# Performance work log

Hardware: AMD Instinct MI355X
Metric: run time of the kernel (lower is better)

The kernel has to match this reference:

```python
import jax, jax.numpy as jnp
import numpy as np

B, C, H, W = 4, 512, 128, 128
CI = C // 2   # inter_planes
CQ = C // 8   # q/k dim in CrossAttention


def conv1x1(x, w, b=None):
    # x: [B,Cin,H,W], w: [Cout,Cin]
    y = jnp.einsum('oc,bchw->bohw', w, x)
    if b is not None:
        y = y + b[None, :, None, None]
    return y


def setup_inputs() -> dict:
    key = jax.random.key(0)
    ks = jax.random.split(key, 13)
    s = 0.05
    return {
        'x': jax.random.normal(ks[0], (B, C, H, W), jnp.float32),
        # SCCA gating params (1x1 convs, no bias except conv_up)
        'w_q_right': jax.random.normal(ks[1], (1, C), jnp.float32) * s,
        'w_v_right': jax.random.normal(ks[2], (CI, C), jnp.float32) * s,
        'w_up': jax.random.normal(ks[3], (C, CI), jnp.float32) * s,
        'b_up': jnp.zeros((C,), jnp.float32),
        'w_q_left': jax.random.normal(ks[4], (CI, C), jnp.float32) * s,
        'w_v_left': jax.random.normal(ks[5], (CI, C), jnp.float32) * s,
        # CrossAttention params (1x1 convs with bias)
        'wq': jax.random.normal(ks[6], (CQ, C), jnp.float32) * s,
        'bq': jnp.zeros((CQ,), jnp.float32),
        'wk': jax.random.normal(ks[7], (CQ, C), jnp.float32) * s,
        'bk': jnp.zeros((CQ,), jnp.float32),
        'wv': jax.random.normal(ks[8], (C, C), jnp.float32) * s,
        'bv': jnp.zeros((C,), jnp.float32),
        'gamma': jnp.asarray(0.5, jnp.float32),
    }


def cross_attention(x, wq, bq, wk, bk, wv, bv, gamma):
    # criss-cross attention: each pixel attends to its row and column
    b, c, h, w = x.shape
    q = conv1x1(x, wq, bq)   # [B,CQ,H,W]
    k = conv1x1(x, wk, bk)   # [B,CQ,H,W]
    v = conv1x1(x, wv, bv)   # [B,C,H,W]
    # column (H) affinities with -inf on the self diagonal (as in INF())
    diag = jnp.where(jnp.eye(h, dtype=bool), -jnp.inf, 0.0).astype(x.dtype)
    e_h = jnp.einsum('bchw,bcgw->bhwg', q, k) + diag[None, :, None, :]  # [B,H,W,H]
    e_w = jnp.einsum('bchw,bchv->bhwv', q, k)                            # [B,H,W,W]
    att = jax.nn.softmax(jnp.concatenate([e_h, e_w], axis=-1), axis=-1)  # [B,H,W,H+W]
    a_h, a_w = att[..., :h], att[..., h:]
    out_h = jnp.einsum('bcgw,bhwg->bchw', v, a_h)
    out_w = jnp.einsum('bchv,bhwv->bchw', v, a_w)
    return gamma * (out_h + out_w) + x


def spatial_weighted(x, w_q_right, w_v_right, w_up, b_up):
    b, c, h, w = x.shape
    input_x = conv1x1(x, w_v_right).reshape(b, CI, h * w)       # [B,CI,HW]
    mask = jax.nn.softmax(conv1x1(x, w_q_right).reshape(b, h * w), axis=-1)  # [B,HW]
    ctx = jnp.einsum('bcn,bn->bc', input_x, mask)               # [B,CI]
    ctx = jnp.einsum('oc,bc->bo', w_up, ctx) + b_up             # [B,C]
    mask_ch = jax.nn.sigmoid(ctx)[:, :, None, None]
    return x * mask_ch


def channel_weighted(x, w_q_left, w_v_left):
    b, c, h, w = x.shape
    g_x = conv1x1(x, w_q_left)                                  # [B,CI,H,W]
    avg = g_x.mean(axis=(2, 3))                                 # [B,CI]
    theta = conv1x1(x, w_v_left).reshape(b, CI, h * w)          # [B,CI,HW]
    ctx = jax.nn.softmax(jnp.einsum('bc,bcn->bn', avg, theta), axis=-1)
    mask_sp = jax.nn.sigmoid(ctx).reshape(b, 1, h, w)
    return x * mask_sp


def reference(x, w_q_right, w_v_right, w_up, b_up, w_q_left, w_v_left,
              wq, bq, wk, bk, wv, bv, gamma):
    cc = spatial_weighted(x, w_q_right, w_v_right, w_up, b_up)
    cc = cross_attention(cc, wq, bq, wk, bk, wv, bv, gamma)
    cs = channel_weighted(x, w_q_left, w_v_left)
    cs = cross_attention(cs, wq, bq, wk, bk, wv, bv, gamma)
    out = cs + cc
    out = cross_attention(out, wq, bq, wk, bk, wv, bv, gamma)
    return out
```

## Files before the change

kernel.cpp:

```cpp
#include <hip/hip_runtime.h>
#include <hip/hip_bf16.h>
#include <math.h>

typedef __hip_bfloat16 bf16;
typedef __attribute__((ext_vector_type(8))) short s16x8;
typedef __attribute__((ext_vector_type(4))) float f32x4;

constexpr int Bn  = 4;
constexpr int Cn  = 512;
constexpr int Hn  = 128;
constexpr int Wn  = 128;
constexpr int Nn  = Hn * Wn;
constexpr int CQn = 64;
constexpr int CIn = 256;

__device__ __forceinline__ float bf2f(bf16 v){ return __bfloat162float(v); }
__device__ __forceinline__ bf16  f2bf(float v){ return __float2bfloat16(v); }

__device__ __forceinline__ void gload_lds16(const void* g, void* l){
  __builtin_amdgcn_global_load_lds(
      (const __attribute__((address_space(1))) unsigned int*)g,
      (__attribute__((address_space(3))) unsigned int*)l,
      16, 0, 0);
}


__global__ __launch_bounds__(256) void k_dotc2(const float* __restrict__ x,
                                               const float* __restrict__ w,
                                               int wstride,
                                               float* __restrict__ part){
  int t = blockIdx.x * 256 + threadIdx.x;
  int half = blockIdx.y;
  int b = t >> 14;
  const float* wp = w + (size_t)b * wstride + half * 256;
  const float* xp = x + (size_t)b * Cn * Nn + (size_t)(half * 256) * Nn + (t & (Nn - 1));
  float acc = 0.f;
  #pragma unroll 16
  for (int c = 0; c < 256; ++c) acc += wp[c] * xp[(size_t)c * Nn];
  part[(size_t)half * (Bn * Nn) + t] = acc;
}

__global__ __launch_bounds__(256) void k_dotcadd(const float* __restrict__ part,
                                                 float* __restrict__ out){
  int t = blockIdx.x * 256 + threadIdx.x;
  out[t] = part[t] + part[(size_t)Bn * Nn + t];
}

__global__ __launch_bounds__(256) void k_rowmean(const float* __restrict__ x,
                                                 float* __restrict__ out,
                                                 float scale){
  int bc = blockIdx.x;
  const float* xp = x + (size_t)bc * Nn;
  float acc = 0.f;
  for (int n = threadIdx.x; n < Nn; n += 256) acc += xp[n];
  for (int o = 32; o > 0; o >>= 1) acc += __shfl_down(acc, o);
  __shared__ float red[4];
  if ((threadIdx.x & 63) == 0) red[threadIdx.x >> 6] = acc;
  __syncthreads();
  if (threadIdx.x == 0) out[bc] = (red[0] + red[1] + red[2] + red[3]) * scale;
}

__global__ __launch_bounds__(256) void k_rowdot(const float* __restrict__ W,
                                                const float* __restrict__ vec,
                                                float* __restrict__ out){
  __shared__ float vs[Cn];
  int b = blockIdx.x, t = threadIdx.x;
  for (int j = t; j < Cn; j += 256) vs[j] = vec[b * Cn + j];
  __syncthreads();
  const float4* wp = (const float4*)(W + (size_t)t * Cn);
  float a = 0.f;
  #pragma unroll 4
  for (int j = 0; j < Cn / 4; ++j){
    float4 w4 = wp[j];
    a += w4.x * vs[4*j] + w4.y * vs[4*j+1] + w4.z * vs[4*j+2] + w4.w * vs[4*j+3];
  }
  out[b * CIn + t] = a;
}

__global__ __launch_bounds__(256) void k_coldot(const float* __restrict__ W,
                                                const float* __restrict__ vec,
                                                float* __restrict__ out){
  __shared__ float vs[CIn];
  int b = blockIdx.y, t = threadIdx.x;
  int c = blockIdx.x * 256 + t;
  if (t < CIn) vs[t] = vec[b * CIn + t];
  __syncthreads();
  float a = 0.f;
  #pragma unroll 8
  for (int j = 0; j < CIn; ++j) a += W[(size_t)j * Cn + c] * vs[j];
  out[b * Cn + c] = a;
}

__global__ __launch_bounds__(256) void k_mch2(const float* __restrict__ w_up,
                                              const float* __restrict__ b_up,
                                              const float* __restrict__ ctx,
                                              float* __restrict__ mch){
  __shared__ float cs[CIn];
  int b = blockIdx.y, t = threadIdx.x;
  int o = blockIdx.x * 256 + t;
  if (t < CIn) cs[t] = ctx[b * CIn + t];
  __syncthreads();
  const float4* wp = (const float4*)(w_up + (size_t)o * CIn);
  float a = b_up[o];
  #pragma unroll 4
  for (int j = 0; j < CIn / 4; ++j){
    float4 w4 = wp[j];
    a += w4.x * cs[4*j] + w4.y * cs[4*j+1] + w4.z * cs[4*j+2] + w4.w * cs[4*j+3];
  }
  mch[b * Cn + o] = 1.f / (1.f + expf(-a));
}

__global__ __launch_bounds__(1024) void k_stats(const float* __restrict__ vv,
                                                float* __restrict__ stats){
  int b = blockIdx.x;
  const float* pp = vv + (size_t)b * Nn;
  int t = threadIdx.x;
  float m = -3.4e38f;
  for (int n = t; n < Nn; n += 1024) m = fmaxf(m, pp[n]);
  for (int o = 32; o > 0; o >>= 1) m = fmaxf(m, __shfl_down(m, o));
  __shared__ float red[16];
  int wid = t >> 6, lid = t & 63;
  if (lid == 0) red[wid] = m;
  __syncthreads();
  if (t == 0){
    float q = red[0];
    for (int i = 1; i < 16; i++) q = fmaxf(q, red[i]);
    red[0] = q;
  }
  __syncthreads();
  m = red[0];
  __syncthreads();
  float s = 0.f;
  for (int n = t; n < Nn; n += 1024) s += expf(pp[n] - m);
  for (int o = 32; o > 0; o >>= 1) s += __shfl_down(s, o);
  if (lid == 0) red[wid] = s;
  __syncthreads();
  if (t == 0){
    float q = 0.f;
    for (int i = 0; i < 16; i++) q += red[i];
    stats[b * 2]     = m;
    stats[b * 2 + 1] = q;
  }
}

__global__ __launch_bounds__(256) void k_weighted(const float* __restrict__ x,
                                                  const float* __restrict__ logits,
                                                  const float* __restrict__ stats,
                                                  float* __restrict__ out){
  int bc = blockIdx.x;
  int b = bc >> 9;
  const float* xp = x + (size_t)bc * Nn;
  const float* lp = logits + (size_t)b * Nn;
  float m = stats[b * 2], den = stats[b * 2 + 1];
  float acc = 0.f;
  for (int n = threadIdx.x; n < Nn; n += 256) acc += xp[n] * expf(lp[n] - m);
  for (int o = 32; o > 0; o >>= 1) acc += __shfl_down(acc, o);
  __shared__ float red[4];
  if ((threadIdx.x & 63) == 0) red[threadIdx.x >> 6] = acc;
  __syncthreads();
  if (threadIdx.x == 0) out[bc] = (red[0] + red[1] + red[2] + red[3]) / den;
}

__global__ __launch_bounds__(256) void k_msp(const float* __restrict__ lg,
                                             const float* __restrict__ stats,
                                             float* __restrict__ msp){
  int t = blockIdx.x * 256 + threadIdx.x;
  int b = t >> 14;
  float v = expf(lg[t] - stats[b * 2]) / stats[b * 2 + 1];
  msp[t] = 1.f / (1.f + expf(-v));
}

__global__ __launch_bounds__(256) void k_applyT3(const float* __restrict__ x,
                                                 const float* __restrict__ mch,
                                                 const float* __restrict__ msp,
                                                 bf16* __restrict__ cc_hi,
                                                 bf16* __restrict__ cc_lo,
                                                 bf16* __restrict__ cs_hi,
                                                 bf16* __restrict__ cs_lo){
  __shared__ bf16 tch[32][33], tcl[32][33], tsh[32][33], tsl[32][33];
  int nt = blockIdx.x, ct = blockIdx.y, b = blockIdx.z;
  int n0 = nt * 32, c0 = ct * 32;
  int t = threadIdx.x;
  #pragma unroll
  for (int kk = 0; kk < 4; ++kk){
    int idx = t + kk * 256;
    int cl = idx >> 5, nl = idx & 31;
    float xv = x[((size_t)(b * Cn + c0 + cl)) * Nn + n0 + nl];
    float ccv = xv * mch[b * Cn + c0 + cl];
    float csv = xv * msp[b * Nn + n0 + nl];
    bf16 h1 = f2bf(ccv);
    tch[cl][nl] = h1;
    tcl[cl][nl] = f2bf(ccv - bf2f(h1));
    bf16 h2 = f2bf(csv);
    tsh[cl][nl] = h2;
    tsl[cl][nl] = f2bf(csv - bf2f(h2));
  }
  __syncthreads();
  #pragma unroll
  for (int kk = 0; kk < 4; ++kk){
    int idx = t + kk * 256;
    int nl = idx >> 5, cl = idx & 31;
    size_t o = ((size_t)(b * Nn + n0 + nl)) * Cn + c0 + cl;
    cc_hi[o] = tch[cl][nl];
    cc_lo[o] = tcl[cl][nl];
    cs_hi[o] = tsh[cl][nl];
    cs_lo[o] = tsl[cl][nl];
  }
}


__global__ __launch_bounds__(256) void k_cvt_w(const float* __restrict__ in,
                                               bf16* __restrict__ out, int n){
  int t = blockIdx.x * 256 + threadIdx.x;
  if (t < n) out[t] = f2bf(in[t]);
}

__global__ __launch_bounds__(256) void k_prep_wqk(const float* __restrict__ wq,
                                                  const float* __restrict__ wk,
                                                  const float* __restrict__ bq,
                                                  const float* __restrict__ bk,
                                                  bf16* __restrict__ wqk_hi,
                                                  bf16* __restrict__ wqk_lo,
                                                  float* __restrict__ bqk){
  int t = blockIdx.x * 256 + threadIdx.x;
  int o = t >> 9, c = t & 511;
  float v = (o < 64) ? wq[(size_t)o * Cn + c] : wk[(size_t)(o - 64) * Cn + c];
  bf16 h = f2bf(v);
  wqk_hi[t] = h;
  wqk_lo[t] = f2bf(v - bf2f(h));
  if (t < 128) bqk[t] = (t < 64) ? bq[t] : bk[t - 64];
}

__global__ __launch_bounds__(256) void k_cvt_T(const float* __restrict__ in,
                                               bf16* __restrict__ out_hi,
                                               bf16* __restrict__ out_lo){
  __shared__ bf16 th_[32][33];
  __shared__ bf16 tl_[32][33];
  int nt = blockIdx.x, ct = blockIdx.y, b = blockIdx.z;
  int n0 = nt * 32, c0 = ct * 32;
  int t = threadIdx.x;
  #pragma unroll
  for (int kk = 0; kk < 4; ++kk){
    int idx = t + kk * 256;
    int cl = idx >> 5, nl = idx & 31;
    float v = in[((size_t)(b * Cn + c0 + cl)) * Nn + n0 + nl];
    bf16 h = f2bf(v);
    th_[cl][nl] = h;
    tl_[cl][nl] = f2bf(v - bf2f(h));
  }
  __syncthreads();
  #pragma unroll
  for (int kk = 0; kk < 4; ++kk){
    int idx = t + kk * 256;
    int nl = idx >> 5, cl = idx & 31;
    size_t o = ((size_t)(b * Nn + n0 + nl)) * Cn + c0 + cl;
    out_hi[o] = th_[cl][nl];
    out_lo[o] = tl_[cl][nl];
  }
}


__global__ __launch_bounds__(256) void k_v_mfma(const bf16* __restrict__ xT,
                                                const bf16* __restrict__ wvb,
                                                const float* __restrict__ bv,
                                                bf16* __restrict__ v){
  __shared__ short As[128 * 64];
  __shared__ short Bs[128 * 64];
  __shared__ float bvs[128];
  int lin = blockIdx.x;
  int swz = (lin & 7) * 256 + (lin >> 3);
  int cb = (swz & 3) * 128;
  int nb = ((swz >> 2) & 127) * 128;
  int b  = swz >> 9;
  int t = threadIdx.x, lane = t & 63, wid = t >> 6;
  int wm = wid >> 1, wn = wid & 1;
  int l15 = lane & 15, l4 = lane >> 4;
  if (t < 128) bvs[t] = bv[cb + t];
  f32x4 acc[4][4];
  #pragma unroll
  for (int i = 0; i < 4; i++)
    #pragma unroll
    for (int j = 0; j < 4; j++) acc[i][j] = (f32x4){0.f, 0.f, 0.f, 0.f};

  const bf16* wp = wvb + (size_t)cb * Cn;
  const bf16* xp = xT + ((size_t)b * Nn + nb) * Cn;
  int r8 = lane >> 3;
  int kc = (lane & 7) * 8;
  for (int kt = 0; kt < 8; ++kt){
    int k0 = kt * 64;
    #pragma unroll
    for (int j = 0; j < 4; ++j){
      int inst = wid * 4 + j;
      int row = inst * 8 + r8;
      gload_lds16(wp + (size_t)row * Cn + k0 + kc, (char*)As + inst * 1024);
      gload_lds16(xp + (size_t)row * Cn + k0 + kc, (char*)Bs + inst * 1024);
    }
    __syncthreads();
    #pragma unroll
    for (int kk = 0; kk < 64; kk += 32){
      s16x8 a[4], bb[4];
      #pragma unroll
      for (int mi = 0; mi < 4; mi++)
        a[mi] = *(const s16x8*)&As[(wm * 64 + mi * 16 + l15) * 64 + kk + l4 * 8];
      #pragma unroll
      for (int ni = 0; ni < 4; ni++)
        bb[ni] = *(const s16x8*)&Bs[(wn * 64 + ni * 16 + l15) * 64 + kk + l4 * 8];
      #pragma unroll
      for (int mi = 0; mi < 4; mi++)
        #pragma unroll
        for (int ni = 0; ni < 4; ni++)
          acc[mi][ni] = __builtin_amdgcn_mfma_f32_16x16x32_bf16(a[mi], bb[ni], acc[mi][ni], 0, 0, 0);
    }
    __syncthreads();
  }
  #pragma unroll
  for (int mi = 0; mi < 4; mi++){
    #pragma unroll
    for (int r = 0; r < 4; r++){
      int cl = wm * 64 + mi * 16 + l4 * 4 + r;
      int c  = cb + cl;
      float bias = bvs[cl];
      #pragma unroll
      for (int ni = 0; ni < 4; ni++){
        int n = nb + wn * 64 + ni * 16 + l15;
        v[((size_t)(b * Cn + c)) * Nn + n] = f2bf(acc[mi][ni][r] + bias);
      }
    }
  }
}

__global__ __launch_bounds__(256) void k_qk_mfma(const bf16* __restrict__ xT_hi,
                                                 const bf16* __restrict__ xT_lo,
                                                 const bf16* __restrict__ wqk_hi,
                                                 const bf16* __restrict__ wqk_lo,
                                                 const float* __restrict__ bqk,
                                                 bf16* __restrict__ qhw,
                                                 bf16* __restrict__ khw){
  __shared__ char smem[65536];
  short* Ah = (short*)smem;
  short* Al = Ah + 8192;
  short* Bh = Al + 8192;
  short* Bl = Bh + 8192;
  char*  Os = smem;
  __shared__ float bs[128];
  int h = blockIdx.x, b = blockIdx.y;
  int nb = h * 128;
  int t = threadIdx.x, lane = t & 63, wid = t >> 6;
  int wm = wid >> 1, wn = wid & 1;
  int l15 = lane & 15, l4 = lane >> 4;
  if (t < 128) bs[t] = bqk[t];
  f32x4 acc[4][4];
  #pragma unroll
  for (int i = 0; i < 4; i++)
    #pragma unroll
    for (int j = 0; j < 4; j++) acc[i][j] = (f32x4){0.f, 0.f, 0.f, 0.f};

  const bf16* xh = xT_hi + ((size_t)b * Nn + nb) * Cn;
  const bf16* xl = xT_lo + ((size_t)b * Nn + nb) * Cn;
  int r8 = lane >> 3;
  int kc = (lane & 7) * 8;
  for (int kt = 0; kt < 8; ++kt){
    int k0 = kt * 64;
    #pragma unroll
    for (int j = 0; j < 4; ++j){
      int inst = wid * 4 + j;
      int row = inst * 8 + r8;
      size_t off = (size_t)row * Cn + k0 + kc;
      gload_lds16(wqk_hi + off, (char*)Ah + inst * 1024);
      gload_lds16(wqk_lo + off, (char*)Al + inst * 1024);
      gload_lds16(xh + off,     (char*)Bh + inst * 1024);
      gload_lds16(xl + off,     (char*)Bl + inst * 1024);
    }
    __syncthreads();
    #pragma unroll
    for (int kk = 0; kk < 64; kk += 32){
      s16x8 ah[4], al[4], bh[4], bl[4];
      #pragma unroll
      for (int mi = 0; mi < 4; mi++){
        int idx = (wm * 64 + mi * 16 + l15) * 64 + kk + l4 * 8;
        ah[mi] = *(const s16x8*)&Ah[idx];
        al[mi] = *(const s16x8*)&Al[idx];
      }
      #pragma unroll
      for (int ni = 0; ni < 4; ni++){
        int idx = (wn * 64 + ni * 16 + l15) * 64 + kk + l4 * 8;
        bh[ni] = *(const s16x8*)&Bh[idx];
        bl[ni] = *(const s16x8*)&Bl[idx];
      }
      #pragma unroll
      for (int mi = 0; mi < 4; mi++)
        #pragma unroll
        for (int ni = 0; ni < 4; ni++){
          acc[mi][ni] = __builtin_amdgcn_mfma_f32_16x16x32_bf16(ah[mi], bh[ni], acc[mi][ni], 0, 0, 0);
          acc[mi][ni] = __builtin_amdgcn_mfma_f32_16x16x32_bf16(ah[mi], bl[ni], acc[mi][ni], 0, 0, 0);
          acc[mi][ni] = __builtin_amdgcn_mfma_f32_16x16x32_bf16(al[mi], bh[ni], acc[mi][ni], 0, 0, 0);
        }
    }
    __syncthreads();
  }
  #pragma unroll
  for (int mi = 0; mi < 4; mi++){
    #pragma unroll
    for (int r = 0; r < 4; r++){
      int o = wm * 64 + mi * 16 + l4 * 4 + r;
      float bias = bs[o];
      #pragma unroll
      for (int ni = 0; ni < 4; ni++){
        int n = wn * 64 + ni * 16 + l15;
        bf16 bv = f2bf(acc[mi][ni][r] + bias);
        int byte = (n * 256 + o * 2) ^ ((n & 7) << 4);
        *(unsigned short*)(Os + byte) = *(unsigned short*)&bv;
      }
    }
  }
  __syncthreads();
  #pragma unroll
  for (int i = 0; i < 8; ++i){
    int s = t + i * 256;
    int row = s >> 3, seg = s & 7;
    int w = row & 127, qk = row >> 7;
    int o0 = qk * 64 + seg * 8;
    int byte = (w * 256 + o0 * 2) ^ ((w & 7) << 4);
    s16x8 d = *(const s16x8*)(Os + byte);
    bf16* dst = (qk == 0 ? qhw : khw) + (((size_t)b * Wn + w) * Hn + h) * CQn + seg * 8;
    *(s16x8*)dst = d;
  }
}


__global__ __launch_bounds__(256) void k_att_h(const bf16* __restrict__ qhw,
                                               const bf16* __restrict__ khw,
                                               const bf16* __restrict__ vT,
                                               float* __restrict__ mh,
                                               float* __restrict__ sh,
                                               bf16* __restrict__ ohX){
  __shared__ char smem[65536];
  char* attb = smem;
  char* vbb  = smem + 32768;
  float* redm = (float*)(smem + 32768);
  float* reds = redm + 256;
  int w = blockIdx.x, b = blockIdx.y;
  int t = threadIdx.x, lane = t & 63, wid = t >> 6;
  int wm = wid >> 1, wn = wid & 1;
  int l15 = lane & 15, l4 = lane >> 4;

  const bf16* qp = qhw + ((size_t)(b * Wn + w)) * (Hn * CQn);
  const bf16* kp = khw + ((size_t)(b * Wn + w)) * (Hn * CQn);
  f32x4 acc[4][4];
  #pragma unroll
  for (int i = 0; i < 4; i++)
    #pragma unroll
    for (int j = 0; j < 4; j++) acc[i][j] = (f32x4){0.f, 0.f, 0.f, 0.f};
  #pragma unroll
  for (int kk = 0; kk < 64; kk += 32){
    s16x8 a[4], bb[4];
    #pragma unroll
    for (int mi = 0; mi < 4; mi++)
      a[mi] = *(const s16x8*)(qp + (size_t)(wm * 64 + mi * 16 + l15) * CQn + kk + l4 * 8);
    #pragma unroll
    for (int ni = 0; ni < 4; ni++)
      bb[ni] = *(const s16x8*)(kp + (size_t)(wn * 64 + ni * 16 + l15) * CQn + kk + l4 * 8);
    #pragma unroll
    for (int mi = 0; mi < 4; mi++)
      #pragma unroll
      for (int ni = 0; ni < 4; ni++)
        acc[mi][ni] = __builtin_amdgcn_mfma_f32_16x16x32_bf16(a[mi], bb[ni], acc[mi][ni], 0, 0, 0);
  }
  if (wm == wn){
    #pragma unroll
    for (int mi = 0; mi < 4; mi++)
      #pragma unroll
      for (int r = 0; r < 4; r++)
        if (l15 == l4 * 4 + r) acc[mi][mi][r] = -1e30f;
  }
  float rm[4][4];
  #pragma unroll
  for (int mi = 0; mi < 4; mi++)
    #pragma unroll
    for (int r = 0; r < 4; r++){
      float m = fmaxf(fmaxf(acc[mi][0][r], acc[mi][1][r]),
                      fmaxf(acc[mi][2][r], acc[mi][3][r]));
      m = fmaxf(m, __shfl_xor(m, 1));
      m = fmaxf(m, __shfl_xor(m, 2));
      m = fmaxf(m, __shfl_xor(m, 4));
      m = fmaxf(m, __shfl_xor(m, 8));
      rm[mi][r] = m;
    }
  if (l15 == 0){
    #pragma unroll
    for (int mi = 0; mi < 4; mi++)
      #pragma unroll
      for (int r = 0; r < 4; r++)
        redm[wn * 128 + wm * 64 + mi * 16 + l4 * 4 + r] = rm[mi][r];
  }
  __syncthreads();
  float rs[4][4];
  #pragma unroll
  for (int mi = 0; mi < 4; mi++)
    #pragma unroll
    for (int r = 0; r < 4; r++){
      int h = wm * 64 + mi * 16 + l4 * 4 + r;
      float m = fmaxf(redm[h], redm[128 + h]);
      rm[mi][r] = m;
      float s = 0.f;
      #pragma unroll
      for (int ni = 0; ni < 4; ni++){
        acc[mi][ni][r] = expf(acc[mi][ni][r] - m);
        s += acc[mi][ni][r];
      }
      s += __shfl_xor(s, 1);
      s += __shfl_xor(s, 2);
      s += __shfl_xor(s, 4);
      s += __shfl_xor(s, 8);
      rs[mi][r] = s;
    }
  if (l15 == 0){
    #pragma unroll
    for (int mi = 0; mi < 4; mi++)
      #pragma unroll
      for (int r = 0; r < 4; r++)
        reds[wn * 128 + wm * 64 + mi * 16 + l4 * 4 + r] = rs[mi][r];
  }
  __syncthreads();
  #pragma unroll
  for (int mi = 0; mi < 4; mi++)
    #pragma unroll
    for (int r = 0; r < 4; r++){
      int h = wm * 64 + mi * 16 + l4 * 4 + r;
      if (wn == 0 && l15 == 0){
        mh[(size_t)(b * Wn + w) * Hn + h] = rm[mi][r];
        sh[(size_t)(b * Wn + w) * Hn + h] = reds[h] + reds[128 + h];
      }
      #pragma unroll
      for (int ni = 0; ni < 4; ni++){
        int g = wn * 64 + ni * 16 + l15;
        bf16 bv = f2bf(acc[mi][ni][r]);
        int byte = (h * 256 + g * 2) ^ ((h & 7) << 4);
        *(unsigned short*)(attb + byte) = *(unsigned short*)&bv;
      }
    }
  __syncthreads();
  for (int cb = 0; cb < Cn; cb += 128){
    const bf16* vp = vT + ((size_t)(b * Wn + w) * Cn + cb) * Hn;
    for (int s = t; s < 2048; s += 256){
      int row = s >> 4, seg = s & 15;
      s16x8 d = *(const s16x8*)(vp + (size_t)row * Hn + seg * 8);
      int byte = (row * 256 + seg * 16) ^ ((row & 7) << 4);
      *(s16x8*)(vbb + byte) = d;
    }
    __syncthreads();
    f32x4 acc2[4][4];
    #pragma unroll
    for (int i = 0; i < 4; i++)
      #pragma unroll
      for (int j = 0; j < 4; j++) acc2[i][j] = (f32x4){0.f, 0.f, 0.f, 0.f};
    #pragma unroll
    for (int kk = 0; kk < 128; kk += 32){
      s16x8 a[4], bb[4];
      #pragma unroll
      for (int mi = 0; mi < 4; mi++){
        int row = wm * 64 + mi * 16 + l15;
        int byte = (row * 256 + (kk + l4 * 8) * 2) ^ ((row & 7) << 4);
        a[mi] = *(const s16x8*)(vbb + byte);
      }
      #pragma unroll
      for (int ni = 0; ni < 4; ni++){
        int row = wn * 64 + ni * 16 + l15;
        int byte = (row * 256 + (kk + l4 * 8) * 2) ^ ((row & 7) << 4);
        bb[ni] = *(const s16x8*)(attb + byte);
      }
      #pragma unroll
      for (int mi = 0; mi < 4; mi++)
        #pragma unroll
        for (int ni = 0; ni < 4; ni++)
          acc2[mi][ni] = __builtin_amdgcn_mfma_f32_16x16x32_bf16(a[mi], bb[ni], acc2[mi][ni], 0, 0, 0);
    }
    bf16* op = ohX + ((size_t)(b * Cn + cb)) * Nn + (size_t)w * Hn;
    #pragma unroll
    for (int mi = 0; mi < 4; mi++)
      #pragma unroll
      for (int r = 0; r < 4; r++){
        int cl = wm * 64 + mi * 16 + l4 * 4 + r;
        #pragma unroll
        for (int ni = 0; ni < 4; ni++){
          int h = wn * 64 + ni * 16 + l15;
          op[(size_t)cl * Nn + h] = f2bf(acc2[mi][ni][r]);
        }
      }
    __syncthreads();
  }
}

__global__ __launch_bounds__(256) void k_att_w(const bf16* __restrict__ qhw,
                                               const bf16* __restrict__ khw,
                                               const bf16* __restrict__ v,
                                               float* __restrict__ mw,
                                               float* __restrict__ sw,
                                               bf16* __restrict__ ow){
  __shared__ char smem[65536];
  char* attb = smem;
  char* vbb  = smem + 32768;
  float* redm = (float*)(smem + 32768);
  float* reds = redm + 256;
  int h = blockIdx.x, b = blockIdx.y;
  int t = threadIdx.x, lane = t & 63, wid = t >> 6;
  int wm = wid >> 1, wn = wid & 1;
  int l15 = lane & 15, l4 = lane >> 4;

  const bf16* qp = qhw + (size_t)b * Wn * Hn * CQn + (size_t)h * CQn;
  const bf16* kp = khw + (size_t)b * Wn * Hn * CQn + (size_t)h * CQn;
  f32x4 acc[4][4];
  #pragma unroll
  for (int i = 0; i < 4; i++)
    #pragma unroll
    for (int j = 0; j < 4; j++) acc[i][j] = (f32x4){0.f, 0.f, 0.f, 0.f};
  #pragma unroll
  for (int kk = 0; kk < 64; kk += 32){
    s16x8 a[4], bb[4];
    #pragma unroll
    for (int mi = 0; mi < 4; mi++)
      a[mi] = *(const s16x8*)(qp + (size_t)(wm * 64 + mi * 16 + l15) * (Hn * CQn) + kk + l4 * 8);
    #pragma unroll
    for (int ni = 0; ni < 4; ni++)
      bb[ni] = *(const s16x8*)(kp + (size_t)(wn * 64 + ni * 16 + l15) * (Hn * CQn) + kk + l4 * 8);
    #pragma unroll
    for (int mi = 0; mi < 4; mi++)
      #pragma unroll
      for (int ni = 0; ni < 4; ni++)
        acc[mi][ni] = __builtin_amdgcn_mfma_f32_16x16x32_bf16(a[mi], bb[ni], acc[mi][ni], 0, 0, 0);
  }
  float rm[4][4];
  #pragma unroll
  for (int mi = 0; mi < 4; mi++)
    #pragma unroll
    for (int r = 0; r < 4; r++){
      float m = fmaxf(fmaxf(acc[mi][0][r], acc[mi][1][r]),
                      fmaxf(acc[mi][2][r], acc[mi][3][r]));
      m = fmaxf(m, __shfl_xor(m, 1));
      m = fmaxf(m, __shfl_xor(m, 2));
      m = fmaxf(m, __shfl_xor(m, 4));
      m = fmaxf(m, __shfl_xor(m, 8));
      rm[mi][r] = m;
    }
  if (l15 == 0){
    #pragma unroll
    for (int mi = 0; mi < 4; mi++)
      #pragma unroll
      for (int r = 0; r < 4; r++)
        redm[wn * 128 + wm * 64 + mi * 16 + l4 * 4 + r] = rm[mi][r];
  }
  __syncthreads();
  float rs[4][4];
  #pragma unroll
  for (int mi = 0; mi < 4; mi++)
    #pragma unroll
    for (int r = 0; r < 4; r++){
      int wr = wm * 64 + mi * 16 + l4 * 4 + r;
      float m = fmaxf(redm[wr], redm[128 + wr]);
      rm[mi][r] = m;
      float s = 0.f;
      #pragma unroll
      for (int ni = 0; ni < 4; ni++){
        acc[mi][ni][r] = expf(acc[mi][ni][r] - m);
        s += acc[mi][ni][r];
      }
      s += __shfl_xor(s, 1);
      s += __shfl_xor(s, 2);
      s += __shfl_xor(s, 4);
      s += __shfl_xor(s, 8);
      rs[mi][r] = s;
    }
  if (l15 == 0){
    #pragma unroll
    for (int mi = 0; mi < 4; mi++)
      #pragma unroll
      for (int r = 0; r < 4; r++)
        reds[wn * 128 + wm * 64 + mi * 16 + l4 * 4 + r] = rs[mi][r];
  }
  __syncthreads();
  #pragma unroll
  for (int mi = 0; mi < 4; mi++)
    #pragma unroll
    for (int r = 0; r < 4; r++){
      int wr = wm * 64 + mi * 16 + l4 * 4 + r;
      if (wn == 0 && l15 == 0){
        mw[(size_t)(b * Hn + h) * Wn + wr] = rm[mi][r];
        sw[(size_t)(b * Hn + h) * Wn + wr] = reds[wr] + reds[128 + wr];
      }
      #pragma unroll
      for (int ni = 0; ni < 4; ni++){
        int g = wn * 64 + ni * 16 + l15;
        bf16 bv = f2bf(acc[mi][ni][r]);
        int byte = (wr * 256 + g * 2) ^ ((wr & 7) << 4);
        *(unsigned short*)(attb + byte) = *(unsigned short*)&bv;
      }
    }
  __syncthreads();
  for (int cb = 0; cb < Cn; cb += 128){
    const bf16* vp = v + (size_t)(b * Cn + cb) * Nn + (size_t)h * Wn;
    for (int s = t; s < 2048; s += 256){
      int row = s >> 4, seg = s & 15;
      s16x8 d = *(const s16x8*)(vp + (size_t)row * Nn + seg * 8);
      int byte = (row * 256 + seg * 16) ^ ((row & 7) << 4);
      *(s16x8*)(vbb + byte) = d;
    }
    __syncthreads();
    f32x4 acc2[4][4];
    #pragma unroll
    for (int i = 0; i < 4; i++)
      #pragma unroll
      for (int j = 0; j < 4; j++) acc2[i][j] = (f32x4){0.f, 0.f, 0.f, 0.f};
    #pragma unroll
    for (int kk = 0; kk < 128; kk += 32){
      s16x8 a[4], bb[4];
      #pragma unroll
      for (int mi = 0; mi < 4; mi++){
        int row = wm * 64 + mi * 16 + l15;
        int byte = (row * 256 + (kk + l4 * 8) * 2) ^ ((row & 7) << 4);
        a[mi] = *(const s16x8*)(vbb + byte);
      }
      #pragma unroll
      for (int ni = 0; ni < 4; ni++){
        int row = wn * 64 + ni * 16 + l15;
        int byte = (row * 256 + (kk + l4 * 8) * 2) ^ ((row & 7) << 4);
        bb[ni] = *(const s16x8*)(attb + byte);
      }
      #pragma unroll
      for (int mi = 0; mi < 4; mi++)
        #pragma unroll
        for (int ni = 0; ni < 4; ni++)
          acc2[mi][ni] = __builtin_amdgcn_mfma_f32_16x16x32_bf16(a[mi], bb[ni], acc2[mi][ni], 0, 0, 0);
    }
    bf16* op = ow + (size_t)(b * Cn + cb) * Nn + (size_t)h * Wn;
    #pragma unroll
    for (int mi = 0; mi < 4; mi++)
      #pragma unroll
      for (int r = 0; r < 4; r++){
        int cl = wm * 64 + mi * 16 + l4 * 4 + r;
        #pragma unroll
        for (int ni = 0; ni < 4; ni++){
          int wr = wn * 64 + ni * 16 + l15;
          op[(size_t)cl * Nn + wr] = f2bf(acc2[mi][ni][r]);
        }
      }
    __syncthreads();
  }
}

__global__ __launch_bounds__(256) void k_alpha(const float* __restrict__ mh,
                                               const float* __restrict__ sh,
                                               const float* __restrict__ mw,
                                               const float* __restrict__ sw,
                                               float* __restrict__ ahT,
                                               float* __restrict__ aw){
  int t = blockIdx.x * 256 + threadIdx.x;
  int b = t >> 14;
  int hw = t & (Nn - 1);
  int h = hw >> 7, w = hw & 127;
  size_t ih = (size_t)(b * Wn + w) * Hn + h;
  size_t iw = t;
  float mhv = mh[ih], mwv = mw[iw];
  float M = fmaxf(mhv, mwv);
  float eh_ = expf(mhv - M), ew_ = expf(mwv - M);
  float inv = 1.f / (sh[ih] * eh_ + sw[iw] * ew_);
  ahT[t] = eh_ * inv;
  aw[t]  = ew_ * inv;
}


__global__ __launch_bounds__(256) void k_trans(const bf16* __restrict__ in,
                                               bf16* __restrict__ out,
                                               int CH){
  __shared__ bf16 tile[32][33];
  int tl = blockIdx.x, c = blockIdx.y, b = blockIdx.z;
  int th = tl >> 2, tw = tl & 3;
  int h0 = th * 32, w0 = tw * 32;
  int t = threadIdx.x;
  const bf16* ip = in + ((size_t)(b * CH + c)) * Nn;
  #pragma unroll
  for (int kk = 0; kk < 4; ++kk){
    int idx = t + kk * 256;
    int hl = idx >> 5, wl = idx & 31;
    tile[hl][wl] = ip[(h0 + hl) * Wn + w0 + wl];
  }
  __syncthreads();
  #pragma unroll
  for (int kk = 0; kk < 4; ++kk){
    int idx = t + kk * 256;
    int wl = idx >> 5, hl = idx & 31;
    out[((size_t)(b * Wn + w0 + wl) * CH + c) * Hn + h0 + hl] = tile[hl][wl];
  }
}

__global__ __launch_bounds__(256) void k_fuse2(const float* __restrict__ in,
                                               const bf16* __restrict__ ohX,
                                               const bf16* __restrict__ ow,
                                               const float* __restrict__ ahT,
                                               const float* __restrict__ aw,
                                               const float* __restrict__ gamma,
                                               float* __restrict__ out){
  __shared__ unsigned short tileT[64][138];
  int c = blockIdx.x, half = blockIdx.y, b = blockIdx.z;
  int t = threadIdx.x;
  float g = gamma[0];
  int h0 = half * 64;
  const bf16* ohp = ohX + ((size_t)(b * Cn + c)) * Nn;
  #pragma unroll
  for (int i = 0; i < 4; ++i){
    int s = t + i * 256;
    int w = s >> 3, seg = s & 7;
    s16x8 d = *(const s16x8*)(ohp + (size_t)w * Hn + h0 + seg * 8);
    #pragma unroll
    for (int j = 0; j < 8; ++j)
      tileT[seg * 8 + j][w] = (unsigned short)d[j];
  }
  __syncthreads();
  size_t base = ((size_t)(b * Cn + c)) * Nn;
  #pragma unroll
  for (int i = 0; i < 8; ++i){
    int o = t + i * 256;
    int hl = o >> 5, w4 = (o & 31) * 4;
    int h = h0 + hl;
    size_t idx = base + (size_t)h * Wn + w4;
    size_t aidx = (size_t)b * Nn + (size_t)h * Wn + w4;
    ushort4 owv = *(const ushort4*)((const unsigned short*)ow + idx);
    float4 ah4 = *(const float4*)(ahT + aidx);
    float4 aw4 = *(const float4*)(aw + aidx);
    float4 inv = in ? *(const float4*)(in + idx) : (float4){0.f,0.f,0.f,0.f};
    float r[4];
    #pragma unroll
    for (int j = 0; j < 4; ++j){
      unsigned short uh = tileT[hl][w4 + j];
      unsigned short uo = ((const unsigned short*)&owv)[j];
      float ohv = bf2f(*(bf16*)&uh);
      float owf = bf2f(*(bf16*)&uo);
      float ahv = ((const float*)&ah4)[j];
      float awv = ((const float*)&aw4)[j];
      r[j] = g * (ahv * ohv + awv * owf) + ((const float*)&inv)[j];
    }
    float4 o4 = { r[0], r[1], r[2], r[3] };
    *(float4*)(out + idx) = o4;
  }
}

__global__ __launch_bounds__(256) void k_fuse3(const float* __restrict__ x,
                                               const float* __restrict__ mch,
                                               const float* __restrict__ msp,
                                               const bf16* __restrict__ oh1,
                                               const bf16* __restrict__ ow1,
                                               const float* __restrict__ a1h,
                                               const float* __restrict__ a1w,
                                               const bf16* __restrict__ oh2,
                                               const bf16* __restrict__ ow2,
                                               const float* __restrict__ a2h,
                                               const float* __restrict__ a2w,
                                               const float* __restrict__ gamma,
                                               float* __restrict__ out){
  __shared__ unsigned short t1[64][138];
  __shared__ unsigned short t2[64][138];
  int c = blockIdx.x, half = blockIdx.y, b = blockIdx.z;
  int t = threadIdx.x;
  float g = gamma[0];
  float mc = mch[b * Cn + c];
  int h0 = half * 64;
  const bf16* p1 = oh1 + ((size_t)(b * Cn + c)) * Nn;
  const bf16* p2 = oh2 + ((size_t)(b * Cn + c)) * Nn;
  #pragma unroll
  for (int i = 0; i < 4; ++i){
    int s = t + i * 256;
    int w = s >> 3, seg = s & 7;
    s16x8 d1 = *(const s16x8*)(p1 + (size_t)w * Hn + h0 + seg * 8);
    s16x8 d2 = *(const s16x8*)(p2 + (size_t)w * Hn + h0 + seg * 8);
    #pragma unroll
    for (int j = 0; j < 8; ++j){
      t1[seg * 8 + j][w] = (unsigned short)d1[j];
      t2[seg * 8 + j][w] = (unsigned short)d2[j];
    }
  }
  __syncthreads();
  size_t base = ((size_t)(b * Cn + c)) * Nn;
  #pragma unroll
  for (int i = 0; i < 8; ++i){
    int o = t + i * 256;
    int hl = o >> 5, w4 = (o & 31) * 4;
    int h = h0 + hl;
    size_t idx = base + (size_t)h * Wn + w4;
    size_t aidx = (size_t)b * Nn + (size_t)h * Wn + w4;
    ushort4 o1v = *(const ushort4*)((const unsigned short*)ow1 + idx);
    ushort4 o2v = *(const ushort4*)((const unsigned short*)ow2 + idx);
    float4 a1h4 = *(const float4*)(a1h + aidx);
    float4 a1w4 = *(const float4*)(a1w + aidx);
    float4 a2h4 = *(const float4*)(a2h + aidx);
    float4 a2w4 = *(const float4*)(a2w + aidx);
    float4 xv4  = *(const float4*)(x + idx);
    float4 mn4  = *(const float4*)(msp + aidx);
    float r[4];
    #pragma unroll
    for (int j = 0; j < 4; ++j){
      unsigned short u1 = t1[hl][w4 + j];
      unsigned short u2 = t2[hl][w4 + j];
      unsigned short w1 = ((const unsigned short*)&o1v)[j];
      unsigned short w2 = ((const unsigned short*)&o2v)[j];
      float oh1v = bf2f(*(bf16*)&u1), ow1v = bf2f(*(bf16*)&w1);
      float oh2v = bf2f(*(bf16*)&u2), ow2v = bf2f(*(bf16*)&w2);
      float term1 = g * (((const float*)&a1h4)[j] * oh1v + ((const float*)&a1w4)[j] * ow1v);
      float term2 = g * (((const float*)&a2h4)[j] * oh2v + ((const float*)&a2w4)[j] * ow2v);
      float resid = ((const float*)&xv4)[j] * (mc + ((const float*)&mn4)[j]);
      r[j] = term2 + resid + term1;
    }
    float4 o4 = { r[0], r[1], r[2], r[3] };
    *(float4*)(out + idx) = o4;
  }
}


static void run_att(const bf16* xT_hi, const bf16* xT_lo,
                    const bf16* wqk_hi, const bf16* wqk_lo, const float* bqk,
                    const bf16* wvb, const float* bv,
                    bf16* qhw, bf16* khw, bf16* v, bf16* vT,
                    float* mh, float* sh, float* mw, float* sw,
                    float* ahT, float* aw, bf16* tmp, hipStream_t stream){
  bf16* ohX = tmp;
  bf16* ow  = tmp + (size_t)Bn * Cn * Nn;
  k_qk_mfma<<<dim3(Nn / 128, Bn), 256, 0, stream>>>(xT_hi, xT_lo, wqk_hi, wqk_lo, bqk,
                                                    qhw, khw);
  k_v_mfma<<<2048, 256, 0, stream>>>(xT_hi, wvb, bv, v);
  k_trans<<<dim3(16, Cn, Bn), 256, 0, stream>>>(v, vT, Cn);
  k_att_h<<<dim3(Wn, Bn), 256, 0, stream>>>(qhw, khw, vT, mh, sh, ohX);
  k_att_w<<<dim3(Hn, Bn), 256, 0, stream>>>(qhw, khw, v, mw, sw, ow);
  k_alpha<<<Bn * Nn / 256, 256, 0, stream>>>(mh, sh, mw, sw, ahT, aw);
}

extern "C" void kernel_launch(void* const* d_in, const int* in_sizes, int n_in,
                              void* d_out, int out_size, void* d_ws, size_t ws_size,
                              hipStream_t stream){
  (void)in_sizes; (void)n_in; (void)out_size; (void)ws_size;
  const float* x         = (const float*)d_in[0];
  const float* w_q_right = (const float*)d_in[1];
  const float* w_v_right = (const float*)d_in[2];
  const float* w_up      = (const float*)d_in[3];
  const float* b_up      = (const float*)d_in[4];
  const float* w_q_left  = (const float*)d_in[5];
  const float* w_v_left  = (const float*)d_in[6];
  const float* wq        = (const float*)d_in[7];
  const float* bq        = (const float*)d_in[8];
  const float* wk        = (const float*)d_in[9];
  const float* bk        = (const float*)d_in[10];
  const float* wv        = (const float*)d_in[11];
  const float* bv        = (const float*)d_in[12];
  const float* gamma     = (const float*)d_in[13];

  const size_t SZ_MAP = (size_t)Bn * Cn * Nn;
  char* p = (char*)d_ws;
  float* buf0   = (float*)p; p += SZ_MAP * 4;
  float* buf1   = (float*)p; p += SZ_MAP * 4;
  bf16*  vbuf   = (bf16*)p;  p += SZ_MAP * 2;
  bf16*  vT     = (bf16*)p;  p += SZ_MAP * 2;
  bf16*  qhw    = (bf16*)p;  p += (size_t)Bn * CQn * Nn * 2;
  bf16*  khw    = (bf16*)p;  p += (size_t)Bn * CQn * Nn * 2;
  float* ebuf   = (float*)p; p += (size_t)SZ_MAP * 2;
  float* logits = (float*)p; p += (size_t)Bn * Nn * 4;
  float* ctxlog = (float*)p; p += (size_t)Bn * Nn * 4;
  float* msp    = (float*)p; p += (size_t)Bn * Nn * 4;
  float* xbar   = (float*)p; p += Bn * Cn * 4;
  float* wgt    = (float*)p; p += Bn * Cn * 4;
  float* u      = (float*)p; p += Bn * Cn * 4;
  float* mch    = (float*)p; p += Bn * Cn * 4;
  float* avg    = (float*)p; p += Bn * CIn * 4;
  float* ctx    = (float*)p; p += Bn * CIn * 4;
  float* stats_sp = (float*)p; p += 64;
  float* stats_ch = (float*)p; p += 64;
  bf16*  wvb    = (bf16*)p;  p += (size_t)Cn * Cn * 2;
  bf16*  wqk_hi = (bf16*)p;  p += (size_t)128 * Cn * 2;
  bf16*  wqk_lo = (bf16*)p;  p += (size_t)128 * Cn * 2;
  float* bqk    = (float*)p; p += 128 * 4;
  float* mh     = (float*)p; p += (size_t)Bn * Nn * 4;
  float* sh     = (float*)p; p += (size_t)Bn * Nn * 4;
  float* mw     = (float*)p; p += (size_t)Bn * Nn * 4;
  float* sw     = (float*)p; p += (size_t)Bn * Nn * 4;
  float* ah1    = (float*)p; p += (size_t)Bn * Nn * 4;
  float* aw1    = (float*)p; p += (size_t)Bn * Nn * 4;
  float* ah2    = (float*)p; p += (size_t)Bn * Nn * 4;
  float* aw2    = (float*)p; p += (size_t)Bn * Nn * 4;
  float* dpart  = (float*)p; p += (size_t)2 * Bn * Nn * 4;

  bf16*  cc_hi  = (bf16*)ebuf;
  bf16*  cc_lo  = (bf16*)d_out;
  bf16*  cs_hi  = (bf16*)buf1;
  bf16*  cs_lo  = (bf16*)buf1 + SZ_MAP;
  bf16*  xT_hi3 = (bf16*)ebuf;
  bf16*  xT_lo3 = (bf16*)d_out;

  k_cvt_w<<<(Cn * Cn + 255) / 256, 256, 0, stream>>>(wv, wvb, Cn * Cn);
  k_prep_wqk<<<(128 * Cn) / 256, 256, 0, stream>>>(wq, wk, bq, bk, wqk_hi, wqk_lo, bqk);

  k_dotc2<<<dim3(Bn * Nn / 256, 2), 256, 0, stream>>>(x, w_q_right, 0, dpart);
  k_dotcadd<<<Bn * Nn / 256, 256, 0, stream>>>(dpart, logits);
  k_rowmean<<<Bn * Cn, 256, 0, stream>>>(x, xbar, 1.f / Nn);
  k_rowdot<<<Bn, 256, 0, stream>>>(w_q_left, xbar, avg);
  k_coldot<<<dim3(Cn / 256, Bn), 256, 0, stream>>>(w_v_left, avg, u);
  k_stats<<<Bn, 1024, 0, stream>>>(logits, stats_sp);
  k_weighted<<<Bn * Cn, 256, 0, stream>>>(x, logits, stats_sp, wgt);
  k_rowdot<<<Bn, 256, 0, stream>>>(w_v_right, wgt, ctx);
  k_mch2<<<dim3(Cn / 256, Bn), 256, 0, stream>>>(w_up, b_up, ctx, mch);
  k_dotc2<<<dim3(Bn * Nn / 256, 2), 256, 0, stream>>>(x, u, Cn, dpart);
  k_dotcadd<<<Bn * Nn / 256, 256, 0, stream>>>(dpart, ctxlog);
  k_stats<<<Bn, 1024, 0, stream>>>(ctxlog, stats_ch);
  k_msp<<<Bn * Nn / 256, 256, 0, stream>>>(ctxlog, stats_ch, msp);

  k_applyT3<<<dim3(Nn / 32, Cn / 32, Bn), 256, 0, stream>>>(x, mch, msp,
                                                            cc_hi, cc_lo, cs_hi, cs_lo);

  run_att(cc_hi, cc_lo, wqk_hi, wqk_lo, bqk, wvb, bv,
          qhw, khw, vbuf, vT, mh, sh, mw, sw, ah1, aw1, (bf16*)d_out, stream);
  run_att(cs_hi, cs_lo, wqk_hi, wqk_lo, bqk, wvb, bv,
          qhw, khw, vbuf, vT, mh, sh, mw, sw, ah2, aw2, (bf16*)buf0, stream);
  k_fuse3<<<dim3(Cn, 2, Bn), 256, 0, stream>>>(x, mch, msp,
                                               (const bf16*)d_out,
                                               (const bf16*)d_out + SZ_MAP, ah1, aw1,
                                               (const bf16*)buf0,
                                               (const bf16*)buf0 + SZ_MAP, ah2, aw2,
                                               gamma, buf1);
  k_cvt_T<<<dim3(Nn / 32, Cn / 32, Bn), 256, 0, stream>>>(buf1, xT_hi3, xT_lo3);
  run_att(xT_hi3, xT_lo3, wqk_hi, wqk_lo, bqk, wvb, bv,
          qhw, khw, vbuf, vT, mh, sh, mw, sw, ah1, aw1, (bf16*)buf0, stream);
  k_fuse2<<<dim3(Cn, 2, Bn), 256, 0, stream>>>(buf1, (const bf16*)buf0,
                                               (const bf16*)buf0 + SZ_MAP, ah1, aw1,
                                               gamma, (float*)d_out);
}
```

Baseline: 1.267 ms.

## Fold channel and spatial masks into weights and epilogue scaling instead of materializing

Instead of building two masked, transposed bf16 copies of x (cc and cs), x is transposed once and both attention branches read it. The channel mask is folded into per-batch q/k/v weights (W·diag(mch)), and the spatial mask becomes a per-pixel scale in the GEMM epilogue before the bias is added. This removes one large transpose-and-split pass and halves the activation traffic for the first two attention branches. In exchange it adds per-batch weight-prep kernels and buffers, and changes k_fuse3 from two to four H-slices per channel. Rounding differs slightly because the mask is now applied in the weights rather than in the activations.

```diff
diff --git a/kernel.cpp b/kernel.cpp
--- a/kernel.cpp
+++ b/kernel.cpp
@@ -170,44 +170,6 @@
   msp[t] = 1.f / (1.f + expf(-v));
 }
 
-__global__ __launch_bounds__(256) void k_applyT3(const float* __restrict__ x,
-                                                 const float* __restrict__ mch,
-                                                 const float* __restrict__ msp,
-                                                 bf16* __restrict__ cc_hi,
-                                                 bf16* __restrict__ cc_lo,
-                                                 bf16* __restrict__ cs_hi,
-                                                 bf16* __restrict__ cs_lo){
-  __shared__ bf16 tch[32][33], tcl[32][33], tsh[32][33], tsl[32][33];
-  int nt = blockIdx.x, ct = blockIdx.y, b = blockIdx.z;
-  int n0 = nt * 32, c0 = ct * 32;
-  int t = threadIdx.x;
-  #pragma unroll
-  for (int kk = 0; kk < 4; ++kk){
-    int idx = t + kk * 256;
-    int cl = idx >> 5, nl = idx & 31;
-    float xv = x[((size_t)(b * Cn + c0 + cl)) * Nn + n0 + nl];
-    float ccv = xv * mch[b * Cn + c0 + cl];
-    float csv = xv * msp[b * Nn + n0 + nl];
-    bf16 h1 = f2bf(ccv);
-    tch[cl][nl] = h1;
-    tcl[cl][nl] = f2bf(ccv - bf2f(h1));
-    bf16 h2 = f2bf(csv);
-    tsh[cl][nl] = h2;
-    tsl[cl][nl] = f2bf(csv - bf2f(h2));
-  }
-  __syncthreads();
-  #pragma unroll
-  for (int kk = 0; kk < 4; ++kk){
-    int idx = t + kk * 256;
-    int nl = idx >> 5, cl = idx & 31;
-    size_t o = ((size_t)(b * Nn + n0 + nl)) * Cn + c0 + cl;
-    cc_hi[o] = tch[cl][nl];
-    cc_lo[o] = tcl[cl][nl];
-    cs_hi[o] = tsh[cl][nl];
-    cs_lo[o] = tsl[cl][nl];
-  }
-}
-
 
 __global__ __launch_bounds__(256) void k_cvt_w(const float* __restrict__ in,
                                                bf16* __restrict__ out, int n){
@@ -231,6 +193,32 @@
   if (t < 128) bqk[t] = (t < 64) ? bq[t] : bk[t - 64];
 }
 
+__global__ __launch_bounds__(256) void k_prep_wqk_mch(const float* __restrict__ wq,
+                                                      const float* __restrict__ wk,
+                                                      const float* __restrict__ mch,
+                                                      bf16* __restrict__ hi,
+                                                      bf16* __restrict__ lo){
+  int t = blockIdx.x * 256 + threadIdx.x;
+  int b = t >> 16;
+  int oc = t & 65535;
+  int o = oc >> 9, c = oc & 511;
+  float w = (o < 64) ? wq[(size_t)o * Cn + c] : wk[(size_t)(o - 64) * Cn + c];
+  float v = w * mch[b * Cn + c];
+  bf16 h = f2bf(v);
+  hi[t] = h;
+  lo[t] = f2bf(v - bf2f(h));
+}
+
+__global__ __launch_bounds__(256) void k_prep_wv_mch(const float* __restrict__ wv,
+                                                     const float* __restrict__ mch,
+                                                     bf16* __restrict__ out){
+  int t = blockIdx.x * 256 + threadIdx.x;
+  int b = t >> 18;
+  int oc = t & 262143;
+  int c = oc & 511;
+  out[t] = f2bf(wv[oc] * mch[b * Cn + c]);
+}
+
 __global__ __launch_bounds__(256) void k_cvt_T(const float* __restrict__ in,
                                                bf16* __restrict__ out_hi,
                                                bf16* __restrict__ out_lo){
@@ -262,7 +250,9 @@
 
 __global__ __launch_bounds__(256) void k_v_mfma(const bf16* __restrict__ xT,
                                                 const bf16* __restrict__ wvb,
+                                                int wstride,
                                                 const float* __restrict__ bv,
+                                                const float* __restrict__ nscale,
                                                 bf16* __restrict__ v){
   __shared__ short As[128 * 64];
   __shared__ short Bs[128 * 64];
@@ -282,7 +272,7 @@
     #pragma unroll
     for (int j = 0; j < 4; j++) acc[i][j] = (f32x4){0.f, 0.f, 0.f, 0.f};
 
-  const bf16* wp = wvb + (size_t)cb * Cn;
+  const bf16* wp = wvb + (size_t)b * wstride + (size_t)cb * Cn;
   const bf16* xp = xT + ((size_t)b * Nn + nb) * Cn;
   int r8 = lane >> 3;
   int kc = (lane & 7) * 8;
@@ -313,6 +303,10 @@
     }
     __syncthreads();
   }
+  float sc[4];
+  #pragma unroll
+  for (int ni = 0; ni < 4; ni++)
+    sc[ni] = nscale ? nscale[(size_t)b * Nn + nb + wn * 64 + ni * 16 + l15] : 1.f;
   #pragma unroll
   for (int mi = 0; mi < 4; mi++){
     #pragma unroll
@@ -323,7 +317,7 @@
       #pragma unroll
       for (int ni = 0; ni < 4; ni++){
         int n = nb + wn * 64 + ni * 16 + l15;
-        v[((size_t)(b * Cn + c)) * Nn + n] = f2bf(acc[mi][ni][r] + bias);
+        v[((size_t)(b * Cn + c)) * Nn + n] = f2bf(acc[mi][ni][r] * sc[ni] + bias);
       }
     }
   }
@@ -333,7 +327,9 @@
                                                  const bf16* __restrict__ xT_lo,
                                                  const bf16* __restrict__ wqk_hi,
                                                  const bf16* __restrict__ wqk_lo,
+                                                 int wstride,
                                                  const float* __restrict__ bqk,
+                                                 const float* __restrict__ nscale,
                                                  bf16* __restrict__ qhw,
                                                  bf16* __restrict__ khw){
   __shared__ char smem[65536];
@@ -355,6 +351,8 @@
     #pragma unroll
     for (int j = 0; j < 4; j++) acc[i][j] = (f32x4){0.f, 0.f, 0.f, 0.f};
 
+  const bf16* wh = wqk_hi + (size_t)b * wstride;
+  const bf16* wl = wqk_lo + (size_t)b * wstride;
   const bf16* xh = xT_hi + ((size_t)b * Nn + nb) * Cn;
   const bf16* xl = xT_lo + ((size_t)b * Nn + nb) * Cn;
   int r8 = lane >> 3;
@@ -366,10 +364,10 @@
       int inst = wid * 4 + j;
       int row = inst * 8 + r8;
       size_t off = (size_t)row * Cn + k0 + kc;
-      gload_lds16(wqk_hi + off, (char*)Ah + inst * 1024);
-      gload_lds16(wqk_lo + off, (char*)Al + inst * 1024);
-      gload_lds16(xh + off,     (char*)Bh + inst * 1024);
-      gload_lds16(xl + off,     (char*)Bl + inst * 1024);
+      gload_lds16(wh + off, (char*)Ah + inst * 1024);
+      gload_lds16(wl + off, (char*)Al + inst * 1024);
+      gload_lds16(xh + off, (char*)Bh + inst * 1024);
+      gload_lds16(xl + off, (char*)Bl + inst * 1024);
     }
     __syncthreads();
     #pragma unroll
@@ -398,6 +396,10 @@
     }
     __syncthreads();
   }
+  float sc[4];
+  #pragma unroll
+  for (int ni = 0; ni < 4; ni++)
+    sc[ni] = nscale ? nscale[(size_t)b * Nn + nb + wn * 64 + ni * 16 + l15] : 1.f;
   #pragma unroll
   for (int mi = 0; mi < 4; mi++){
     #pragma unroll
@@ -407,7 +409,7 @@
       #pragma unroll
       for (int ni = 0; ni < 4; ni++){
         int n = wn * 64 + ni * 16 + l15;
-        bf16 bv = f2bf(acc[mi][ni][r] + bias);
+        bf16 bv = f2bf(acc[mi][ni][r] * sc[ni] + bias);
         int byte = (n * 256 + o * 2) ^ ((n & 7) << 4);
         *(unsigned short*)(Os + byte) = *(unsigned short*)&bv;
       }
@@ -856,19 +858,19 @@
                                                const float* __restrict__ a2w,
                                                const float* __restrict__ gamma,
                                                float* __restrict__ out){
-  __shared__ unsigned short t1[64][138];
-  __shared__ unsigned short t2[64][138];
-  int c = blockIdx.x, half = blockIdx.y, b = blockIdx.z;
+  __shared__ unsigned short t1[32][138];
+  __shared__ unsigned short t2[32][138];
+  int c = blockIdx.x, quarter = blockIdx.y, b = blockIdx.z;
   int t = threadIdx.x;
   float g = gamma[0];
   float mc = mch[b * Cn + c];
-  int h0 = half * 64;
+  int h0 = quarter * 32;
   const bf16* p1 = oh1 + ((size_t)(b * Cn + c)) * Nn;
   const bf16* p2 = oh2 + ((size_t)(b * Cn + c)) * Nn;
   #pragma unroll
-  for (int i = 0; i < 4; ++i){
+  for (int i = 0; i < 2; ++i){
     int s = t + i * 256;
-    int w = s >> 3, seg = s & 7;
+    int w = s >> 2, seg = s & 3;
     s16x8 d1 = *(const s16x8*)(p1 + (size_t)w * Hn + h0 + seg * 8);
     s16x8 d2 = *(const s16x8*)(p2 + (size_t)w * Hn + h0 + seg * 8);
     #pragma unroll
@@ -880,7 +882,7 @@
   __syncthreads();
   size_t base = ((size_t)(b * Cn + c)) * Nn;
   #pragma unroll
-  for (int i = 0; i < 8; ++i){
+  for (int i = 0; i < 4; ++i){
     int o = t + i * 256;
     int hl = o >> 5, w4 = (o & 31) * 4;
     int h = h0 + hl;
@@ -915,16 +917,19 @@
 
 
 static void run_att(const bf16* xT_hi, const bf16* xT_lo,
-                    const bf16* wqk_hi, const bf16* wqk_lo, const float* bqk,
-                    const bf16* wvb, const float* bv,
+                    const bf16* wqk_hi, const bf16* wqk_lo, int wqk_bstride,
+                    const float* bqk,
+                    const bf16* wvb, int wv_bstride, const float* bv,
+                    const float* nscale,
                     bf16* qhw, bf16* khw, bf16* v, bf16* vT,
                     float* mh, float* sh, float* mw, float* sw,
                     float* ahT, float* aw, bf16* tmp, hipStream_t stream){
   bf16* ohX = tmp;
   bf16* ow  = tmp + (size_t)Bn * Cn * Nn;
-  k_qk_mfma<<<dim3(Nn / 128, Bn), 256, 0, stream>>>(xT_hi, xT_lo, wqk_hi, wqk_lo, bqk,
+  k_qk_mfma<<<dim3(Nn / 128, Bn), 256, 0, stream>>>(xT_hi, xT_lo, wqk_hi, wqk_lo,
+                                                    wqk_bstride, bqk, nscale,
                                                     qhw, khw);
-  k_v_mfma<<<2048, 256, 0, stream>>>(xT_hi, wvb, bv, v);
+  k_v_mfma<<<2048, 256, 0, stream>>>(xT_hi, wvb, wv_bstride, bv, nscale, v);
   k_trans<<<dim3(16, Cn, Bn), 256, 0, stream>>>(v, vT, Cn);
   k_att_h<<<dim3(Wn, Bn), 256, 0, stream>>>(qhw, khw, vT, mh, sh, ohX);
   k_att_w<<<dim3(Hn, Bn), 256, 0, stream>>>(qhw, khw, v, mw, sw, ow);
@@ -983,16 +988,18 @@
   float* ah2    = (float*)p; p += (size_t)Bn * Nn * 4;
   float* aw2    = (float*)p; p += (size_t)Bn * Nn * 4;
   float* dpart  = (float*)p; p += (size_t)2 * Bn * Nn * 4;
-
-  bf16*  cc_hi  = (bf16*)ebuf;
-  bf16*  cc_lo  = (bf16*)d_out;
-  bf16*  cs_hi  = (bf16*)buf1;
-  bf16*  cs_lo  = (bf16*)buf1 + SZ_MAP;
+  bf16*  wqk_mch_hi = (bf16*)p; p += (size_t)Bn * 128 * Cn * 2;
+  bf16*  wqk_mch_lo = (bf16*)p; p += (size_t)Bn * 128 * Cn * 2;
+  bf16*  wv_mch     = (bf16*)p; p += (size_t)Bn * Cn * Cn * 2;
+
+  bf16*  xT_hi  = (bf16*)ebuf;
+  bf16*  xT_lo  = (bf16*)buf1;
   bf16*  xT_hi3 = (bf16*)ebuf;
   bf16*  xT_lo3 = (bf16*)d_out;
 
   k_cvt_w<<<(Cn * Cn + 255) / 256, 256, 0, stream>>>(wv, wvb, Cn * Cn);
   k_prep_wqk<<<(128 * Cn) / 256, 256, 0, stream>>>(wq, wk, bq, bk, wqk_hi, wqk_lo, bqk);
+  k_cvt_T<<<dim3(Nn / 32, Cn / 32, Bn), 256, 0, stream>>>(x, xT_hi, xT_lo);
 
   k_dotc2<<<dim3(Bn * Nn / 256, 2), 256, 0, stream>>>(x, w_q_right, 0, dpart);
   k_dotcadd<<<Bn * Nn / 256, 256, 0, stream>>>(dpart, logits);
@@ -1003,26 +1010,27 @@
   k_weighted<<<Bn * Cn, 256, 0, stream>>>(x, logits, stats_sp, wgt);
   k_rowdot<<<Bn, 256, 0, stream>>>(w_v_right, wgt, ctx);
   k_mch2<<<dim3(Cn / 256, Bn), 256, 0, stream>>>(w_up, b_up, ctx, mch);
+  k_prep_wqk_mch<<<(Bn * 128 * Cn) / 256, 256, 0, stream>>>(wq, wk, mch,
+                                                            wqk_mch_hi, wqk_mch_lo);
+  k_prep_wv_mch<<<(Bn * Cn * Cn) / 256, 256, 0, stream>>>(wv, mch, wv_mch);
   k_dotc2<<<dim3(Bn * Nn / 256, 2), 256, 0, stream>>>(x, u, Cn, dpart);
   k_dotcadd<<<Bn * Nn / 256, 256, 0, stream>>>(dpart, ctxlog);
   k_stats<<<Bn, 1024, 0, stream>>>(ctxlog, stats_ch);
   k_msp<<<Bn * Nn / 256, 256, 0, stream>>>(ctxlog, stats_ch, msp);
 
-  k_applyT3<<<dim3(Nn / 32, Cn / 32, Bn), 256, 0, stream>>>(x, mch, msp,
-                                                            cc_hi, cc_lo, cs_hi, cs_lo);
-
-  run_att(cc_hi, cc_lo, wqk_hi, wqk_lo, bqk, wvb, bv,
+  run_att(xT_hi, xT_lo, wqk_mch_hi, wqk_mch_lo, 128 * Cn, bqk,
+          wv_mch, Cn * Cn, bv, nullptr,
           qhw, khw, vbuf, vT, mh, sh, mw, sw, ah1, aw1, (bf16*)d_out, stream);
-  run_att(cs_hi, cs_lo, wqk_hi, wqk_lo, bqk, wvb, bv,
+  run_att(xT_hi, xT_lo, wqk_hi, wqk_lo, 0, bqk, wvb, 0, bv, msp,
           qhw, khw, vbuf, vT, mh, sh, mw, sw, ah2, aw2, (bf16*)buf0, stream);
-  k_fuse3<<<dim3(Cn, 2, Bn), 256, 0, stream>>>(x, mch, msp,
+  k_fuse3<<<dim3(Cn, 4, Bn), 256, 0, stream>>>(x, mch, msp,
                                                (const bf16*)d_out,
                                                (const bf16*)d_out + SZ_MAP, ah1, aw1,
                                                (const bf16*)buf0,
                                                (const bf16*)buf0 + SZ_MAP, ah2, aw2,
                                                gamma, buf1);
   k_cvt_T<<<dim3(Nn / 32, Cn / 32, Bn), 256, 0, stream>>>(buf1, xT_hi3, xT_lo3);
-  run_att(xT_hi3, xT_lo3, wqk_hi, wqk_lo, bqk, wvb, bv,
+  run_att(xT_hi3, xT_lo3, wqk_hi, wqk_lo, 0, bqk, wvb, 0, bv, nullptr,
           qhw, khw, vbuf, vT, mh, sh, mw, sw, ah1, aw1, (bf16*)buf0, stream);
   k_fuse2<<<dim3(Cn, 2, Bn), 256, 0, stream>>>(buf1, (const bf16*)buf0,
                                                (const bf16*)buf0 + SZ_MAP, ah1, aw1,
```

New measurement: 1.237 ms. 2.3% less time.
